# Kernel optimization log

Measured on AMD Instinct MI355X. Metric: run time of the kernel, lower is better.

The kernel has to match this reference:

```python
import jax, jax.numpy as jnp
import numpy as np

ZERO_RATIO = 0.7
BATCH = 16384
UNITS = 4096


def setup_inputs() -> dict:
    key = jax.random.key(0)
    X = jax.random.normal(key, (BATCH, UNITS), dtype=jnp.float32)
    return {"X": X}


def reference(X):
    # idx-th smallest activation per row is the threshold (ascending sort)
    idx = int(ZERO_RATIO * X.shape[1])  # static python int
    theta = jnp.sort(X, axis=1)[:, idx]  # [B]
    mask = X >= theta[:, None]
    return X * mask
```

## Files before the change

kernel.cpp:

```cpp
#include <hip/hip_runtime.h>
#include <stdint.h>

#define UNITS  4096
#define CAP    320
#define NSLOT  5
#define LOF    0.44f
#define HIF    0.61f
#define SELBITS 22

__device__ __forceinline__ void lds_barrier() {
    asm volatile("s_waitcnt lgkmcnt(0)" ::: "memory");
    __builtin_amdgcn_s_barrier();
}
__device__ __forceinline__ uint32_t flipu(uint32_t b) {
    return b ^ (uint32_t)(((int32_t)b >> 31) | (int32_t)0x80000000);
}
__device__ __forceinline__ uint32_t mbcnt64(uint64_t m) {
    return __builtin_amdgcn_mbcnt_hi((uint32_t)(m >> 32),
           __builtin_amdgcn_mbcnt_lo((uint32_t)m, 0u));
}

__global__ __launch_bounds__(256, 8) void ksparse_select_kernel(
        const float* __restrict__ X, float* __restrict__ out, int kidx) {
    __shared__ uint32_t list[CAP];
    __shared__ uint32_t cnt;
    __shared__ uint32_t wnb[4];
    __shared__ uint32_t fbc[4];

    const int t    = threadIdx.x;
    const int w    = t >> 6;
    const int lane = t & 63;

    if (t == 0) cnt = 0u;

    float f[16];
    {
        const float4* Xv = reinterpret_cast<const float4*>(X + (size_t)blockIdx.x * UNITS);
#pragma unroll
        for (int j = 0; j < 4; ++j) {
            float4 v = Xv[j * 256 + t];
            f[4*j] = v.x; f[4*j+1] = v.y; f[4*j+2] = v.z; f[4*j+3] = v.w;
        }
    }

    lds_barrier();

    uint64_t mwin[16];
    uint32_t nbw = 0, wtot = 0;
#pragma unroll
    for (int e = 0; e < 16; ++e) {
        const uint64_t mlo = __ballot(f[e] < LOF);
        const uint64_t mhi = __ballot(f[e] < HIF);
        mwin[e] = mhi & ~mlo;
        nbw  += (uint32_t)__popcll(mlo);
        wtot += (uint32_t)__popcll(mwin[e]);
    }
    if (lane == 0) wnb[w] = nbw;

    const uint32_t LOu = __float_as_uint(LOF);
    uint32_t base = 0;
    if (lane == 0) base = atomicAdd(&cnt, wtot);
    base = __shfl(base, 0);
    uint32_t pfx = 0;
#pragma unroll
    for (int e = 0; e < 16; ++e) {
        if (mwin[e] & (1ull << lane)) {
            const uint32_t idx = base + pfx + mbcnt64(mwin[e]);
            if (idx < CAP) list[idx] = __float_as_uint(f[e]) - LOu;
        }
        pfx += (uint32_t)__popcll(mwin[e]);
    }

    lds_barrier();

    const uint32_t c  = cnt;
    const uint32_t cb = wnb[0] + wnb[1] + wnb[2] + wnb[3];
    const uint32_t k  = (uint32_t)kidx;

    float4* Ov = reinterpret_cast<float4*>(out + (size_t)blockIdx.x * UNITS);

    if (cb <= k && k < cb + c && c <= CAP) {
        const uint32_t r = k - cb;

        uint32_t sv[NSLOT];
#pragma unroll
        for (int i = 0; i < NSLOT; ++i) {
            const uint32_t ix = (uint32_t)lane + 64u * i;
            sv[i] = (ix < c) ? list[ix] : 0xFFFFFFFFu;
        }

        uint32_t p = 0;
#pragma unroll
        for (int b = SELBITS - 1; b >= 0; --b) {
            const uint32_t mid = p | (1u << b);
            uint32_t cm = 0;
#pragma unroll
            for (int i = 0; i < NSLOT; ++i)
                cm += (uint32_t)__popcll(__ballot(sv[i] < mid));
            if (cm <= r) p = mid;
        }
        const float th = __uint_as_float(LOu + p);

#pragma unroll
        for (int j = 0; j < 4; ++j) {
            float4 o;
            o.x = (f[4*j]   >= th) ? f[4*j]   : 0.0f;
            o.y = (f[4*j+1] >= th) ? f[4*j+1] : 0.0f;
            o.z = (f[4*j+2] >= th) ? f[4*j+2] : 0.0f;
            o.w = (f[4*j+3] >= th) ? f[4*j+3] : 0.0f;
            Ov[j * 256 + t] = o;
        }
    } else {
        uint32_t p = 0;
#pragma unroll 1
        for (int b = 31; b >= 0; --b) {
            const uint32_t mid = p | (1u << b);
            uint32_t cw = 0;
#pragma unroll
            for (int e = 0; e < 16; ++e)
                cw += (uint32_t)__popcll(__ballot(flipu(__float_as_uint(f[e])) < mid));
            if (lane == 0) fbc[w] = cw;
            lds_barrier();
            const uint32_t cm = fbc[0] + fbc[1] + fbc[2] + fbc[3];
            if (cm <= k) p = mid;
            lds_barrier();
        }
#pragma unroll
        for (int j = 0; j < 4; ++j) {
            float4 o;
            o.x = (flipu(__float_as_uint(f[4*j]))   >= p) ? f[4*j]   : 0.0f;
            o.y = (flipu(__float_as_uint(f[4*j+1])) >= p) ? f[4*j+1] : 0.0f;
            o.z = (flipu(__float_as_uint(f[4*j+2])) >= p) ? f[4*j+2] : 0.0f;
            o.w = (flipu(__float_as_uint(f[4*j+3])) >= p) ? f[4*j+3] : 0.0f;
            Ov[j * 256 + t] = o;
        }
    }
}

extern "C" void kernel_launch(void* const* d_in, const int* in_sizes, int n_in,
                              void* d_out, int out_size, void* d_ws, size_t ws_size,
                              hipStream_t stream) {
    const float* X = (const float*)d_in[0];
    float* out = (float*)d_out;
    const int rows = in_sizes[0] / UNITS;
    const int kidx = (int)(0.7 * UNITS);
    ksparse_select_kernel<<<rows, 256, 0, stream>>>(X, out, kidx);
}
```

Measured before the change: 99.66 us.

## Use per-wave candidate segments and radix-4 selection instead of shared atomic counter

Each wave now writes its window candidates into its own fixed LDS segment, using its running ballot prefix. This replaces the shared atomicAdd counter, the initial barrier and the second pass over the masks. The in-window binary search also moves from radix-2 to radix-4: it resolves two bits per step with three ballot comparisons, which halves the serial dependency chain but adds more ballots per step. The price is a per-wave capacity of 96, so rows with uneven spread across waves fall back to the slow full-bit search more often.

```diff
diff --git a/kernel.cpp b/kernel.cpp
--- a/kernel.cpp
+++ b/kernel.cpp
@@ -2,8 +2,9 @@
 #include <stdint.h>
 
 #define UNITS  4096
-#define CAP    320
-#define NSLOT  5
+#define SEG    96
+#define CAP    (4 * SEG)
+#define NSLOT  6
 #define LOF    0.44f
 #define HIF    0.61f
 #define SELBITS 22
@@ -23,15 +24,13 @@
 __global__ __launch_bounds__(256, 8) void ksparse_select_kernel(
         const float* __restrict__ X, float* __restrict__ out, int kidx) {
     __shared__ uint32_t list[CAP];
-    __shared__ uint32_t cnt;
     __shared__ uint32_t wnb[4];
+    __shared__ uint32_t wc[4];
     __shared__ uint32_t fbc[4];
 
     const int t    = threadIdx.x;
     const int w    = t >> 6;
     const int lane = t & 63;
-
-    if (t == 0) cnt = 0u;
 
     float f[16];
     {
@@ -43,61 +42,68 @@
         }
     }
 
-    lds_barrier();
-
-    uint64_t mwin[16];
-    uint32_t nbw = 0, wtot = 0;
+    const uint32_t LOu = __float_as_uint(LOF);
+    uint32_t nbw = 0, pfx = 0;
 #pragma unroll
     for (int e = 0; e < 16; ++e) {
-        const uint64_t mlo = __ballot(f[e] < LOF);
-        const uint64_t mhi = __ballot(f[e] < HIF);
-        mwin[e] = mhi & ~mlo;
-        nbw  += (uint32_t)__popcll(mlo);
-        wtot += (uint32_t)__popcll(mwin[e]);
+        const bool lo = f[e] < LOF;
+        const bool hi = f[e] < HIF;
+        const uint64_t mlo  = __ballot(lo);
+        const uint64_t mwin = __ballot(hi && !lo);
+        nbw += (uint32_t)__popcll(mlo);
+        if (hi && !lo) {
+            const uint32_t off = pfx + mbcnt64(mwin);
+            if (off < SEG) list[SEG * w + off] = __float_as_uint(f[e]) - LOu;
+        }
+        pfx += (uint32_t)__popcll(mwin);
     }
-    if (lane == 0) wnb[w] = nbw;
-
-    const uint32_t LOu = __float_as_uint(LOF);
-    uint32_t base = 0;
-    if (lane == 0) base = atomicAdd(&cnt, wtot);
-    base = __shfl(base, 0);
-    uint32_t pfx = 0;
-#pragma unroll
-    for (int e = 0; e < 16; ++e) {
-        if (mwin[e] & (1ull << lane)) {
-            const uint32_t idx = base + pfx + mbcnt64(mwin[e]);
-            if (idx < CAP) list[idx] = __float_as_uint(f[e]) - LOu;
-        }
-        pfx += (uint32_t)__popcll(mwin[e]);
-    }
+    if (lane == 0) { wnb[w] = nbw; wc[w] = pfx; }
 
     lds_barrier();
 
-    const uint32_t c  = cnt;
+    const uint32_t c0 = wc[0], c1 = wc[1], c2 = wc[2], c3 = wc[3];
+    const uint32_t c  = c0 + c1 + c2 + c3;
     const uint32_t cb = wnb[0] + wnb[1] + wnb[2] + wnb[3];
     const uint32_t k  = (uint32_t)kidx;
+    const uint32_t mx = max(max(c0, c1), max(c2, c3));
 
     float4* Ov = reinterpret_cast<float4*>(out + (size_t)blockIdx.x * UNITS);
 
-    if (cb <= k && k < cb + c && c <= CAP) {
+    if (cb <= k && k < cb + c && mx <= SEG) {
         const uint32_t r = k - cb;
 
         uint32_t sv[NSLOT];
+        {
+            const bool loh = lane < 32;
+            uint32_t segi[NSLOT], offi[NSLOT];
+            segi[0] = 0;             offi[0] = lane;
+            segi[1] = loh ? 0 : 1;   offi[1] = loh ? 64 + lane : lane - 32;
+            segi[2] = 1;             offi[2] = 32 + lane;
+            segi[3] = 2;             offi[3] = lane;
+            segi[4] = loh ? 2 : 3;   offi[4] = loh ? 64 + lane : lane - 32;
+            segi[5] = 3;             offi[5] = 32 + lane;
 #pragma unroll
-        for (int i = 0; i < NSLOT; ++i) {
-            const uint32_t ix = (uint32_t)lane + 64u * i;
-            sv[i] = (ix < c) ? list[ix] : 0xFFFFFFFFu;
+            for (int i = 0; i < NSLOT; ++i)
+                sv[i] = (offi[i] < wc[segi[i]]) ? list[SEG * segi[i] + offi[i]]
+                                                : 0xFFFFFFFFu;
         }
 
         uint32_t p = 0;
 #pragma unroll
-        for (int b = SELBITS - 1; b >= 0; --b) {
-            const uint32_t mid = p | (1u << b);
-            uint32_t cm = 0;
+        for (int rb = SELBITS - 2; rb >= 0; rb -= 2) {
+            const uint32_t m1 = p | (1u << rb);
+            const uint32_t m2 = p | (2u << rb);
+            const uint32_t m3 = p | (3u << rb);
+            uint32_t n1 = 0, n2 = 0, n3 = 0;
 #pragma unroll
-            for (int i = 0; i < NSLOT; ++i)
-                cm += (uint32_t)__popcll(__ballot(sv[i] < mid));
-            if (cm <= r) p = mid;
+            for (int i = 0; i < NSLOT; ++i) {
+                n1 += (uint32_t)__popcll(__ballot(sv[i] < m1));
+                n2 += (uint32_t)__popcll(__ballot(sv[i] < m2));
+                n3 += (uint32_t)__popcll(__ballot(sv[i] < m3));
+            }
+            if (n3 <= r)      p = m3;
+            else if (n2 <= r) p = m2;
+            else if (n1 <= r) p = m1;
         }
         const float th = __uint_as_float(LOu + p);
 
```

Result: no change. 101.2 us (+1.5%).
